# Optimization experiments

Measured on AMD Instinct MI355X. Metric: run time of the kernel, lower is better.

The kernel has to match this reference:

```python
import jax, jax.numpy as jnp
import numpy as np

B, C, H, W = 64, 3, 512, 512
MIN = 0.33  # min crop fraction from __init__


def setup_inputs() -> dict:
    key = jax.random.key(0)
    k1, k2, k3, k4, k5 = jax.random.split(key, 5)
    img = jax.random.normal(k1, (B, C, H, W), jnp.float32)
    # Replicate the module's internal randint sampling for the crop boxes.
    min_h, min_w = int(MIN * H), int(MIN * W)
    hight = jax.random.randint(k2, (B,), min_h, H)
    width = jax.random.randint(k3, (B,), min_w, W)
    yc = jax.random.randint(k4, (B,), min_h // 2, H)
    xc = jax.random.randint(k5, (B,), min_w // 2, W)
    y1 = jnp.clip(yc - hight // 2, 0, H).astype(jnp.int32)
    y2 = jnp.clip(yc + hight // 2, 0, H).astype(jnp.int32)
    x1 = jnp.clip(xc - width // 2, 0, W).astype(jnp.int32)
    x2 = jnp.clip(xc + width // 2, 0, W).astype(jnp.int32)
    return {"img": img, "y1": y1, "y2": y2, "x1": x1, "x2": x2}


def _axis_coords(start, end, out_size):
    # Source coords for bilinear resize, align_corners=False (torch default).
    n = (end - start).astype(jnp.float32)  # crop length along this axis
    s = (jnp.arange(out_size, dtype=jnp.float32) + 0.5) * n / out_size - 0.5
    s = jnp.clip(s, 0.0, n - 1.0)
    i0 = jnp.floor(s).astype(jnp.int32)
    i1 = jnp.minimum(i0 + 1, end - start - 1)
    wgt = s - i0.astype(jnp.float32)
    return start + i0, start + i1, wgt  # absolute indices into the full image


def _resize_one(img_b, y1, y2, x1, x2):
    # img_b: [C, H, W]; crop [y1:y2, x1:x2] then bilinear-resize back to (H, W)
    iy0, iy1, wy = _axis_coords(y1, y2, H)
    ix0, ix1, wx = _axis_coords(x1, x2, W)
    r0 = jnp.take(img_b, iy0, axis=1)
    r1 = jnp.take(img_b, iy1, axis=1)
    rows = r0 + (r1 - r0) * wy[None, :, None]      # [C, H, W] rows interpolated
    c0 = jnp.take(rows, ix0, axis=2)
    c1 = jnp.take(rows, ix1, axis=2)
    return c0 + (c1 - c0) * wx[None, None, :]      # [C, H, W]


def reference(img, y1, y2, x1, x2):
    return jax.vmap(_resize_one)(img, y1, y2, x1, x2)
```

## Files before the change

### kernel.cpp

```cpp
#include <hip/hip_runtime.h>


#define BB 64
#define CC 3
#define HH 512
#define WW 512

__global__ __launch_bounds__(256) void rand_crop_resize_kernel(
    const float* __restrict__ img,
    const int* __restrict__ y1a, const int* __restrict__ y2a,
    const int* __restrict__ x1a, const int* __restrict__ x2a,
    float* __restrict__ out)
{
    const int row = blockIdx.x;
    const int oy  = row & (HH - 1);
    const int bc  = row >> 9;
    const int c   = bc % CC;
    const int b   = bc / CC;

    const int Y1 = y1a[b], Y2 = y2a[b], X1 = x1a[b], X2 = x2a[b];

    const int   ny_i = Y2 - Y1;
    const float ny   = (float)ny_i;
    float sy = ((float)oy + 0.5f) * ny * (1.0f / 512.0f) - 0.5f;
    sy = fminf(fmaxf(sy, 0.0f), ny - 1.0f);
    int iy0 = (int)floorf(sy);
    int iy1 = min(iy0 + 1, ny_i - 1);
    const float wy = sy - (float)iy0;
    iy0 += Y1;
    iy1 += Y1;

    const size_t plane = ((size_t)(b * CC + c)) * (size_t)HH;
    const float* __restrict__ row0 = img + (plane + (size_t)iy0) * (size_t)WW;
    const float* __restrict__ row1 = img + (plane + (size_t)iy1) * (size_t)WW;

    const int   nx_i  = X2 - X1;
    const float nx    = (float)nx_i;
    const int   nxm1  = nx_i - 1;
    const float nxm1f = nx - 1.0f;

    const int t = threadIdx.x;
    float2 res;

    #pragma unroll
    for (int k = 0; k < 2; ++k) {
        const int ox = 2 * t + k;
        float sx = ((float)ox + 0.5f) * nx * (1.0f / 512.0f) - 0.5f;
        sx = fminf(fmaxf(sx, 0.0f), nxm1f);
        int ix0 = (int)floorf(sx);
        int ix1 = min(ix0 + 1, nxm1);
        const float wx = sx - (float)ix0;
        ix0 += X1;
        ix1 += X1;

        const float v00 = row0[ix0];
        const float v01 = row0[ix1];
        const float v10 = row1[ix0];
        const float v11 = row1[ix1];

        const float r0 = v00 + (v10 - v00) * wy;
        const float r1 = v01 + (v11 - v01) * wy;
        const float v  = r0 + (r1 - r0) * wx;
        if (k == 0) res.x = v; else res.y = v;
    }

    float2* __restrict__ orow = (float2*)(out + (size_t)row * (size_t)WW);
    orow[t] = res;
}

extern "C" void kernel_launch(void* const* d_in, const int* in_sizes, int n_in,
                              void* d_out, int out_size, void* d_ws, size_t ws_size,
                              hipStream_t stream) {
    const float* img = (const float*)d_in[0];
    const int*   y1  = (const int*)d_in[1];
    const int*   y2  = (const int*)d_in[2];
    const int*   x1  = (const int*)d_in[3];
    const int*   x2  = (const int*)d_in[4];
    float*       out = (float*)d_out;

    dim3 grid(BB * CC * HH);
    dim3 block(256);
    hipLaunchKernelGGL(rand_crop_resize_kernel, grid, block, 0, stream,
                       img, y1, y2, x1, x2, out);
}
```

Before: 389.7 us.

## Stage source rows in LDS and remap blocks for XCD-local L2 reuse

Each block now loads the two full source rows into shared memory with coalesced float4 loads, then does the bilinear gathers from LDS rather than scattered global loads. Block indices are also remapped so that each of the 8 XCDs handles a contiguous range of output rows, which keeps neighbouring rows that reuse the same source rows within one L2. The cost is a shared-memory staging step and a barrier, and full rows are read even when the crop is narrower than the image.

```diff
diff --git a/kernel.cpp b/kernel.cpp
--- a/kernel.cpp
+++ b/kernel.cpp
@@ -5,6 +5,8 @@
 #define CC 3
 #define HH 512
 #define WW 512
+#define NROWS (BB * CC * HH)
+#define ROWS_PER_XCD (NROWS / 8)
 
 __global__ __launch_bounds__(256) void rand_crop_resize_kernel(
     const float* __restrict__ img,
@@ -12,36 +14,44 @@
     const int* __restrict__ x1a, const int* __restrict__ x2a,
     float* __restrict__ out)
 {
-    const int row = blockIdx.x;
+    __shared__ float s0[WW];
+    __shared__ float s1[WW];
+
+    const int row = (blockIdx.x & 7) * ROWS_PER_XCD + (blockIdx.x >> 3);
+
     const int oy  = row & (HH - 1);
     const int bc  = row >> 9;
-    const int c   = bc % CC;
     const int b   = bc / CC;
 
     const int Y1 = y1a[b], Y2 = y2a[b], X1 = x1a[b], X2 = x2a[b];
 
     const int   ny_i = Y2 - Y1;
-    const float ny   = (float)ny_i;
-    float sy = ((float)oy + 0.5f) * ny * (1.0f / 512.0f) - 0.5f;
-    sy = fminf(fmaxf(sy, 0.0f), ny - 1.0f);
+    float sy = ((float)oy + 0.5f) * (float)ny_i * (1.0f / 512.0f) - 0.5f;
+    sy = fminf(fmaxf(sy, 0.0f), (float)ny_i - 1.0f);
     int iy0 = (int)floorf(sy);
     int iy1 = min(iy0 + 1, ny_i - 1);
     const float wy = sy - (float)iy0;
     iy0 += Y1;
     iy1 += Y1;
 
-    const size_t plane = ((size_t)(b * CC + c)) * (size_t)HH;
-    const float* __restrict__ row0 = img + (plane + (size_t)iy0) * (size_t)WW;
-    const float* __restrict__ row1 = img + (plane + (size_t)iy1) * (size_t)WW;
+    const size_t plane = (size_t)bc * (size_t)(HH * WW);
+    const float* __restrict__ row0 = img + plane + (size_t)iy0 * (size_t)WW;
+    const float* __restrict__ row1 = img + plane + (size_t)iy1 * (size_t)WW;
+
+    const int t = threadIdx.x;
+    if (t < 128) {
+        ((float4*)s0)[t] = ((const float4*)row0)[t];
+    } else {
+        ((float4*)s1)[t - 128] = ((const float4*)row1)[t - 128];
+    }
+    __syncthreads();
 
     const int   nx_i  = X2 - X1;
     const float nx    = (float)nx_i;
     const int   nxm1  = nx_i - 1;
     const float nxm1f = nx - 1.0f;
 
-    const int t = threadIdx.x;
     float2 res;
-
     #pragma unroll
     for (int k = 0; k < 2; ++k) {
         const int ox = 2 * t + k;
@@ -53,10 +63,10 @@
         ix0 += X1;
         ix1 += X1;
 
-        const float v00 = row0[ix0];
-        const float v01 = row0[ix1];
-        const float v10 = row1[ix0];
-        const float v11 = row1[ix1];
+        const float v00 = s0[ix0];
+        const float v01 = s0[ix1];
+        const float v10 = s1[ix0];
+        const float v11 = s1[ix1];
 
         const float r0 = v00 + (v10 - v00) * wy;
         const float r1 = v01 + (v11 - v01) * wy;
@@ -78,7 +88,7 @@
     const int*   x2  = (const int*)d_in[4];
     float*       out = (float*)d_out;
 
-    dim3 grid(BB * CC * HH);
+    dim3 grid(NROWS);
     dim3 block(256);
     hipLaunchKernelGGL(rand_crop_resize_kernel, grid, block, 0, stream,
                        img, y1, y2, x1, x2, out);
```

Result: faster. 354.3 us (-9.1%).
